# Optimization experiments

Hardware: AMD Instinct MI355X
Metric: run time of the kernel (lower is better)

Reference implementation:

```python
import jax, jax.numpy as jnp
import numpy as np

SCALE = 1.0
DENSE = 4
ITERS = 5


def setup_inputs() -> dict:
    key = jax.random.key(0)
    k1, k2, k3 = jax.random.split(key, 3)
    N, C, H, W = 32, 3, 512, 512
    data = jax.random.uniform(k1, (N, C, H, W), dtype=jnp.float32)
    # marginal attention distributions along x (width) and y (height); strictly positive
    attx = jax.random.uniform(k2, (N, W, 1), dtype=jnp.float32) + 1e-3
    atty = jax.random.uniform(k3, (N, H, 1), dtype=jnp.float32) + 1e-3
    return {"data": data, "attx": attx, "atty": atty}


def _iterative_clip(ax, ay, out_size, dense, iters):
    # ax, ay: (N, A) positive marginals. Normalize so each sums to out_size,
    # then iteratively clip peaks to a threshold and redistribute the clipped
    # mass uniformly (the mobula AttSamplerGrid iterative refinement).
    A = ax.shape[1]
    ax = ax / jnp.sum(ax, 1, keepdims=True) * out_size
    ay = ay / jnp.sum(ay, 1, keepdims=True) * out_size
    thr0 = jnp.float32(dense * out_size / A)
    for i in range(iters):
        t = jnp.minimum(jnp.max(ax, 1, keepdims=True), jnp.max(ay, 1, keepdims=True))
        if i == 0:
            t = jnp.minimum(t, thr0)
        ax = jnp.minimum(ax, t)
        ay = jnp.minimum(ay, t)
        ax = ax + (out_size - jnp.sum(ax, 1, keepdims=True)) / A
        ay = ay + (out_size - jnp.sum(ay, 1, keepdims=True)) / A
    return ax, ay


def _inverse_cdf(att, out_size):
    # att: (N, A) density summing (approximately) to out_size.
    # For each of out_size equally-spaced mass targets, find the fractional
    # source index p (piecewise-linear inverse of the cumulative sum), then
    # map p in [0, A] to a normalized grid coordinate in [-1, 1].
    N, A = att.shape
    c = jnp.cumsum(att, axis=1)                               # (N, A)
    step = c[:, -1] / out_size                                # ~1.0 per output pixel
    t = (jnp.arange(out_size, dtype=att.dtype) + 0.5) * step[:, None]  # (N, out)
    j = jax.vmap(lambda cr, tr: jnp.searchsorted(cr, tr, side="left"))(c, t)
    j = jnp.clip(j, 0, A - 1)
    c_prev = jnp.where(j > 0, jnp.take_along_axis(c, jnp.maximum(j - 1, 0), 1), 0.0)
    dens = jnp.take_along_axis(c, j, 1) - c_prev              # = att[n, j]
    p = j.astype(att.dtype) + (t - c_prev) / jnp.maximum(dens, 1e-6)
    return 2.0 * p / A - 1.0                                  # (N, out) in [-1, 1]


def _grid_sample_bilinear(data, grid):
    # data: (N, C, H, W); grid: (N, Ho, Wo, 2) with grid[...,0]=x, grid[...,1]=y
    # in [-1, 1]; bilinear, align_corners=True, border clamp (grid stays in range).
    N, C, H, W = data.shape
    ix = (grid[..., 0] + 1.0) * 0.5 * (W - 1)
    iy = (grid[..., 1] + 1.0) * 0.5 * (H - 1)
    x0 = jnp.floor(ix)
    y0 = jnp.floor(iy)
    wx = ix - x0
    wy = iy - y0
    x0i = jnp.clip(x0.astype(jnp.int32), 0, W - 1)
    x1i = jnp.clip(x0i + 1, 0, W - 1)
    y0i = jnp.clip(y0.astype(jnp.int32), 0, H - 1)
    y1i = jnp.clip(y0i + 1, 0, H - 1)

    def sample_one(img, x0i, x1i, y0i, y1i, wx, wy):
        # img: (C, H, W); index arrays: (Ho, Wo) -> gathers are (C, Ho, Wo)
        v00 = img[:, y0i, x0i]
        v01 = img[:, y0i, x1i]
        v10 = img[:, y1i, x0i]
        v11 = img[:, y1i, x1i]
        top = v00 * (1.0 - wx) + v01 * wx
        bot = v10 * (1.0 - wx) + v11 * wx
        return top * (1.0 - wy) + bot * wy

    return jax.vmap(sample_one)(data, x0i, x1i, y0i, y1i, wx, wy)


def reference(data, attx, atty):
    N, C, H, W = data.shape
    out_size = int(H * SCALE)
    ax, ay = _iterative_clip(attx[:, :, 0], atty[:, :, 0], out_size, DENSE, ITERS)
    px = _inverse_cdf(ax, out_size)   # x coords, vary along width
    py = _inverse_cdf(ay, out_size)   # y coords, vary along height
    gx = jnp.broadcast_to(px[:, None, :], (N, out_size, out_size))
    gy = jnp.broadcast_to(py[:, :, None], (N, out_size, out_size))
    grid = jnp.stack([gx, gy], axis=3)            # (N, Ho, Wo, 2)
    sampled = _grid_sample_bilinear(data, grid)   # (N, C, Ho, Wo)
    return sampled, grid
```

## Files before the change

kernel.cpp:

```cpp
#include <hip/hip_runtime.h>

#define NB   32
#define NC   3
#define HH   512
#define WW   512
#define AA   512
#define OUT  512

__device__ __forceinline__ void wave_sum2(float& x, float& y) {
#pragma unroll
    for (int m = 32; m > 0; m >>= 1) {
        x += __shfl_xor(x, m, 64);
        y += __shfl_xor(y, m, 64);
    }
}
__device__ __forceinline__ void wave_max2(float& x, float& y) {
#pragma unroll
    for (int m = 32; m > 0; m >>= 1) {
        x = fmaxf(x, __shfl_xor(x, m, 64));
        y = fmaxf(y, __shfl_xor(y, m, 64));
    }
}

__device__ __forceinline__ void block_sum2(float& vx, float& vy,
                                           float* redx, float* redy, int tid) {
    wave_sum2(vx, vy);
    if ((tid & 63) == 0) { redx[tid >> 6] = vx; redy[tid >> 6] = vy; }
    __syncthreads();
    float rx = redx[0], ry = redy[0];
#pragma unroll
    for (int k = 1; k < 8; ++k) { rx += redx[k]; ry += redy[k]; }
    __syncthreads();
    vx = rx; vy = ry;
}
__device__ __forceinline__ void block_max2(float& vx, float& vy,
                                           float* redx, float* redy, int tid) {
    wave_max2(vx, vy);
    if ((tid & 63) == 0) { redx[tid >> 6] = vx; redy[tid >> 6] = vy; }
    __syncthreads();
    float rx = redx[0], ry = redy[0];
#pragma unroll
    for (int k = 1; k < 8; ++k) { rx = fmaxf(rx, redx[k]); ry = fmaxf(ry, redy[k]); }
    __syncthreads();
    vx = rx; vy = ry;
}

__global__ __launch_bounds__(512) void clip_cdf_kernel(
    const float* __restrict__ attx, const float* __restrict__ atty,
    float* __restrict__ px, float* __restrict__ py)
{
    __shared__ float redx[8], redy[8];
    __shared__ float csx[AA], csy[AA];

    const int n    = blockIdx.x;
    const int tid  = threadIdx.x;
    const int wave = tid >> 6;
    const int lane = tid & 63;

    float ax = attx[n * AA + tid];
    float ay = atty[n * AA + tid];

    float sx = ax, sy = ay;
    block_sum2(sx, sy, redx, redy, tid);
    ax = ax / sx * (float)OUT;
    ay = ay / sy * (float)OUT;

#pragma unroll
    for (int it = 0; it < 5; ++it) {
        float mx = ax, my = ay;
        block_max2(mx, my, redx, redy, tid);
        float tv = fminf(mx, my);
        if (it == 0) tv = fminf(tv, 4.0f);
        ax = fminf(ax, tv);
        ay = fminf(ay, tv);
        float sax = ax, say = ay;
        block_sum2(sax, say, redx, redy, tid);
        ax += ((float)OUT - sax) * (1.0f / (float)AA);
        ay += ((float)OUT - say) * (1.0f / (float)AA);
    }

    float vsx = ax, vsy = ay;
#pragma unroll
    for (int off = 1; off < 64; off <<= 1) {
        float ux = __shfl_up(vsx, off, 64);
        float uy = __shfl_up(vsy, off, 64);
        if (lane >= off) { vsx += ux; vsy += uy; }
    }
    if (lane == 63) { redx[wave] = vsx; redy[wave] = vsy; }
    __syncthreads();
    float pfx = 0.0f, pfy = 0.0f;
#pragma unroll
    for (int k = 0; k < 8; ++k) {
        if (k < wave) { pfx += redx[k]; pfy += redy[k]; }
    }
    csx[tid] = vsx + pfx;
    csy[tid] = vsy + pfy;
    __syncthreads();

    const float totx = csx[AA - 1];
    const float toty = csy[AA - 1];
    const float tkx  = ((float)tid + 0.5f) * (totx * (1.0f / (float)OUT));
    const float tky  = ((float)tid + 0.5f) * (toty * (1.0f / (float)OUT));

    {
        int lo = 0, hi = AA;
        while (lo < hi) {
            int mid = (lo + hi) >> 1;
            if (csx[mid] < tkx) lo = mid + 1; else hi = mid;
        }
        int j = min(lo, AA - 1);
        float cprev = (j > 0) ? csx[j - 1] : 0.0f;
        float dens  = csx[j] - cprev;
        float p     = (float)j + (tkx - cprev) / fmaxf(dens, 1e-6f);
        px[n * OUT + tid] = 2.0f * p * (1.0f / (float)AA) - 1.0f;
    }
    {
        int lo = 0, hi = AA;
        while (lo < hi) {
            int mid = (lo + hi) >> 1;
            if (csy[mid] < tky) lo = mid + 1; else hi = mid;
        }
        int j = min(lo, AA - 1);
        float cprev = (j > 0) ? csy[j - 1] : 0.0f;
        float dens  = csy[j] - cprev;
        float p     = (float)j + (tky - cprev) / fmaxf(dens, 1e-6f);
        py[n * OUT + tid] = 2.0f * p * (1.0f / (float)AA) - 1.0f;
    }
}

__global__ __launch_bounds__(256) void sample_kernel(
    const float* __restrict__ data, const float* __restrict__ px,
    const float* __restrict__ py, float* __restrict__ sampled,
    float2* __restrict__ grid)
{
    __shared__ float lrow[6][WW];

    const int d = blockIdx.x;
    const int g = ((d & 7) << 11) + (d >> 3);
    const int n = g >> 9;
    const int i = g & (OUT - 1);

    const float gy  = py[n * OUT + i];
    const float iy  = (gy + 1.0f) * 0.5f * (float)(HH - 1);
    const float y0f = floorf(iy);
    const float wy  = iy - y0f;
    int y0 = (int)y0f;
    y0 = max(0, min(y0, HH - 1));
    const int y1 = min(y0 + 1, HH - 1);

    const float* dbase = data + (size_t)n * NC * HH * WW;

#pragma unroll
    for (int k = 0; k < 3; ++k) {
        const int idx = threadIdx.x + k * 256;
        const int row = idx >> 7;
        const int q   = idx & 127;
        const int c   = (row < 3) ? row : row - 3;
        const int y   = (row < 3) ? y0 : y1;
        const float4 v = ((const float4*)(dbase + ((size_t)c * HH + y) * WW))[q];
        ((float4*)&lrow[row][0])[q] = v;
    }
    __syncthreads();

    float*  sbase  = sampled + (size_t)n * NC * HH * WW + (size_t)i * WW;
    float4* gbase4 = (float4*)(grid + ((size_t)n * OUT + i) * OUT);
    const float omwy = 1.0f - wy;

    const int t = threadIdx.x;
    const float2 pxv = ((const float2*)(px + n * OUT))[t];

    const float ixa  = (pxv.x + 1.0f) * 0.5f * (float)(WW - 1);
    const float x0fa = floorf(ixa);
    const float wxa  = ixa - x0fa;
    int x0a = (int)x0fa; x0a = max(0, min(x0a, WW - 1));
    const int x1a = min(x0a + 1, WW - 1);
    const float omwxa = 1.0f - wxa;
    const float ixb  = (pxv.y + 1.0f) * 0.5f * (float)(WW - 1);
    const float x0fb = floorf(ixb);
    const float wxb  = ixb - x0fb;
    int x0b = (int)x0fb; x0b = max(0, min(x0b, WW - 1));
    const int x1b = min(x0b + 1, WW - 1);
    const float omwxb = 1.0f - wxb;

    gbase4[t] = make_float4(pxv.x, gy, pxv.y, gy);

#pragma unroll
    for (int c = 0; c < NC; ++c) {
        const float* r0 = &lrow[c][0];
        const float* r1 = &lrow[3 + c][0];
        const float topa = r0[x0a] * omwxa + r0[x1a] * wxa;
        const float bota = r1[x0a] * omwxa + r1[x1a] * wxa;
        const float topb = r0[x0b] * omwxb + r0[x1b] * wxb;
        const float botb = r1[x0b] * omwxb + r1[x1b] * wxb;
        const float ra = topa * omwy + bota * wy;
        const float rb = topb * omwy + botb * wy;
        ((float2*)(sbase + (size_t)c * HH * WW))[t] = make_float2(ra, rb);
    }
}

extern "C" void kernel_launch(void* const* d_in, const int* in_sizes, int n_in,
                              void* d_out, int out_size, void* d_ws, size_t ws_size,
                              hipStream_t stream) {
    const float* data = (const float*)d_in[0];
    const float* attx = (const float*)d_in[1];
    const float* atty = (const float*)d_in[2];

    float* px = (float*)d_ws;
    float* py = px + NB * OUT;

    float*  out     = (float*)d_out;
    float*  sampled = out;
    float2* grid    = (float2*)(out + (size_t)NB * NC * HH * WW);

    clip_cdf_kernel<<<NB, 512, 0, stream>>>(attx, atty, px, py);
    sample_kernel<<<NB * OUT, 256, 0, stream>>>(data, px, py, sampled, grid);
}
```

Baseline: 253.8 us.

## Use single-wave clip/CDF kernel and per-channel thread mapping in sampler

The clip/CDF preprocessing kernel becomes a single 64-lane wave in which each lane holds 8 elements. Reductions and the prefix scan then need only shuffles, which removes the block-level barriers, but each lane now runs 16 serial binary searches. The sample kernel goes from 256 to 384 threads so that each thread handles one channel and four output pixels, writing sampled values as float4. The grid write moves to the first 256 threads. The aim is to cut barrier latency in the small kernel and widen the stores in the bandwidth-bound sampler.

```diff
diff --git a/kernel.cpp b/kernel.cpp
--- a/kernel.cpp
+++ b/kernel.cpp
@@ -7,128 +7,134 @@
 #define AA   512
 #define OUT  512
 
-__device__ __forceinline__ void wave_sum2(float& x, float& y) {
-#pragma unroll
-    for (int m = 32; m > 0; m >>= 1) {
-        x += __shfl_xor(x, m, 64);
-        y += __shfl_xor(y, m, 64);
-    }
-}
-__device__ __forceinline__ void wave_max2(float& x, float& y) {
-#pragma unroll
-    for (int m = 32; m > 0; m >>= 1) {
-        x = fmaxf(x, __shfl_xor(x, m, 64));
-        y = fmaxf(y, __shfl_xor(y, m, 64));
-    }
-}
-
-__device__ __forceinline__ void block_sum2(float& vx, float& vy,
-                                           float* redx, float* redy, int tid) {
-    wave_sum2(vx, vy);
-    if ((tid & 63) == 0) { redx[tid >> 6] = vx; redy[tid >> 6] = vy; }
-    __syncthreads();
-    float rx = redx[0], ry = redy[0];
-#pragma unroll
-    for (int k = 1; k < 8; ++k) { rx += redx[k]; ry += redy[k]; }
-    __syncthreads();
-    vx = rx; vy = ry;
-}
-__device__ __forceinline__ void block_max2(float& vx, float& vy,
-                                           float* redx, float* redy, int tid) {
-    wave_max2(vx, vy);
-    if ((tid & 63) == 0) { redx[tid >> 6] = vx; redy[tid >> 6] = vy; }
-    __syncthreads();
-    float rx = redx[0], ry = redy[0];
-#pragma unroll
-    for (int k = 1; k < 8; ++k) { rx = fmaxf(rx, redx[k]); ry = fmaxf(ry, redy[k]); }
-    __syncthreads();
-    vx = rx; vy = ry;
-}
-
-__global__ __launch_bounds__(512) void clip_cdf_kernel(
+__global__ __launch_bounds__(64) void clip_cdf_wave(
     const float* __restrict__ attx, const float* __restrict__ atty,
     float* __restrict__ px, float* __restrict__ py)
 {
-    __shared__ float redx[8], redy[8];
     __shared__ float csx[AA], csy[AA];
-
     const int n    = blockIdx.x;
-    const int tid  = threadIdx.x;
-    const int wave = tid >> 6;
-    const int lane = tid & 63;
-
-    float ax = attx[n * AA + tid];
-    float ay = atty[n * AA + tid];
-
-    float sx = ax, sy = ay;
-    block_sum2(sx, sy, redx, redy, tid);
-    ax = ax / sx * (float)OUT;
-    ay = ay / sy * (float)OUT;
+    const int lane = threadIdx.x;
+
+    float ax[8], ay[8];
+    {
+        const float4* ap = (const float4*)(attx + n * AA);
+        const float4* bp = (const float4*)(atty + n * AA);
+        float4 a0 = ap[lane * 2], a1 = ap[lane * 2 + 1];
+        float4 b0 = bp[lane * 2], b1 = bp[lane * 2 + 1];
+        ax[0]=a0.x; ax[1]=a0.y; ax[2]=a0.z; ax[3]=a0.w;
+        ax[4]=a1.x; ax[5]=a1.y; ax[6]=a1.z; ax[7]=a1.w;
+        ay[0]=b0.x; ay[1]=b0.y; ay[2]=b0.z; ay[3]=b0.w;
+        ay[4]=b1.x; ay[5]=b1.y; ay[6]=b1.z; ay[7]=b1.w;
+    }
+
+    float sx = 0.0f, sy = 0.0f;
+#pragma unroll
+    for (int j = 0; j < 8; ++j) { sx += ax[j]; sy += ay[j]; }
+#pragma unroll
+    for (int m = 32; m > 0; m >>= 1) {
+        sx += __shfl_xor(sx, m, 64);
+        sy += __shfl_xor(sy, m, 64);
+    }
+    const float scx = (float)OUT / sx;
+    const float scy = (float)OUT / sy;
+#pragma unroll
+    for (int j = 0; j < 8; ++j) { ax[j] *= scx; ay[j] *= scy; }
 
 #pragma unroll
     for (int it = 0; it < 5; ++it) {
-        float mx = ax, my = ay;
-        block_max2(mx, my, redx, redy, tid);
+        float mx = ax[0], my = ay[0];
+#pragma unroll
+        for (int j = 1; j < 8; ++j) { mx = fmaxf(mx, ax[j]); my = fmaxf(my, ay[j]); }
+#pragma unroll
+        for (int m = 32; m > 0; m >>= 1) {
+            mx = fmaxf(mx, __shfl_xor(mx, m, 64));
+            my = fmaxf(my, __shfl_xor(my, m, 64));
+        }
         float tv = fminf(mx, my);
         if (it == 0) tv = fminf(tv, 4.0f);
-        ax = fminf(ax, tv);
-        ay = fminf(ay, tv);
-        float sax = ax, say = ay;
-        block_sum2(sax, say, redx, redy, tid);
-        ax += ((float)OUT - sax) * (1.0f / (float)AA);
-        ay += ((float)OUT - say) * (1.0f / (float)AA);
-    }
-
-    float vsx = ax, vsy = ay;
+        float sax = 0.0f, say = 0.0f;
+#pragma unroll
+        for (int j = 0; j < 8; ++j) {
+            ax[j] = fminf(ax[j], tv);  sax += ax[j];
+            ay[j] = fminf(ay[j], tv);  say += ay[j];
+        }
+#pragma unroll
+        for (int m = 32; m > 0; m >>= 1) {
+            sax += __shfl_xor(sax, m, 64);
+            say += __shfl_xor(say, m, 64);
+        }
+        const float dx = ((float)OUT - sax) * (1.0f / (float)AA);
+        const float dy = ((float)OUT - say) * (1.0f / (float)AA);
+#pragma unroll
+        for (int j = 0; j < 8; ++j) { ax[j] += dx; ay[j] += dy; }
+    }
+
+    float psx[8], psy[8];
+    float tx = 0.0f, ty = 0.0f;
+#pragma unroll
+    for (int j = 0; j < 8; ++j) {
+        tx += ax[j]; psx[j] = tx;
+        ty += ay[j]; psy[j] = ty;
+    }
+    float inx = tx, iny = ty;
 #pragma unroll
     for (int off = 1; off < 64; off <<= 1) {
-        float ux = __shfl_up(vsx, off, 64);
-        float uy = __shfl_up(vsy, off, 64);
-        if (lane >= off) { vsx += ux; vsy += uy; }
-    }
-    if (lane == 63) { redx[wave] = vsx; redy[wave] = vsy; }
+        float ux = __shfl_up(inx, off, 64);
+        float uy = __shfl_up(iny, off, 64);
+        if (lane >= off) { inx += ux; iny += uy; }
+    }
+    const float exx = inx - tx;
+    const float exy = iny - ty;
+    const float totx = __shfl(inx, 63, 64);
+    const float toty = __shfl(iny, 63, 64);
+
+    ((float4*)csx)[lane * 2]     = make_float4(exx+psx[0], exx+psx[1], exx+psx[2], exx+psx[3]);
+    ((float4*)csx)[lane * 2 + 1] = make_float4(exx+psx[4], exx+psx[5], exx+psx[6], exx+psx[7]);
+    ((float4*)csy)[lane * 2]     = make_float4(exy+psy[0], exy+psy[1], exy+psy[2], exy+psy[3]);
+    ((float4*)csy)[lane * 2 + 1] = make_float4(exy+psy[4], exy+psy[5], exy+psy[6], exy+psy[7]);
     __syncthreads();
-    float pfx = 0.0f, pfy = 0.0f;
-#pragma unroll
-    for (int k = 0; k < 8; ++k) {
-        if (k < wave) { pfx += redx[k]; pfy += redy[k]; }
-    }
-    csx[tid] = vsx + pfx;
-    csy[tid] = vsy + pfy;
-    __syncthreads();
-
-    const float totx = csx[AA - 1];
-    const float toty = csy[AA - 1];
-    const float tkx  = ((float)tid + 0.5f) * (totx * (1.0f / (float)OUT));
-    const float tky  = ((float)tid + 0.5f) * (toty * (1.0f / (float)OUT));
-
-    {
-        int lo = 0, hi = AA;
-        while (lo < hi) {
-            int mid = (lo + hi) >> 1;
-            if (csx[mid] < tkx) lo = mid + 1; else hi = mid;
-        }
-        int j = min(lo, AA - 1);
-        float cprev = (j > 0) ? csx[j - 1] : 0.0f;
-        float dens  = csx[j] - cprev;
-        float p     = (float)j + (tkx - cprev) / fmaxf(dens, 1e-6f);
-        px[n * OUT + tid] = 2.0f * p * (1.0f / (float)AA) - 1.0f;
-    }
-    {
-        int lo = 0, hi = AA;
-        while (lo < hi) {
-            int mid = (lo + hi) >> 1;
-            if (csy[mid] < tky) lo = mid + 1; else hi = mid;
-        }
-        int j = min(lo, AA - 1);
-        float cprev = (j > 0) ? csy[j - 1] : 0.0f;
-        float dens  = csy[j] - cprev;
-        float p     = (float)j + (tky - cprev) / fmaxf(dens, 1e-6f);
-        py[n * OUT + tid] = 2.0f * p * (1.0f / (float)AA) - 1.0f;
-    }
+
+    const float stx = totx * (1.0f / (float)OUT);
+    const float sty = toty * (1.0f / (float)OUT);
+
+    float outx[8], outy[8];
+#pragma unroll
+    for (int j = 0; j < 8; ++j) {
+        const int t = lane * 8 + j;
+        {
+            const float tk = ((float)t + 0.5f) * stx;
+            int lo = 0, hi = AA;
+            while (lo < hi) {
+                int mid = (lo + hi) >> 1;
+                if (csx[mid] < tk) lo = mid + 1; else hi = mid;
+            }
+            int jj = min(lo, AA - 1);
+            float cprev = (jj > 0) ? csx[jj - 1] : 0.0f;
+            float dens  = csx[jj] - cprev;
+            float p     = (float)jj + (tk - cprev) / fmaxf(dens, 1e-6f);
+            outx[j] = 2.0f * p * (1.0f / (float)AA) - 1.0f;
+        }
+        {
+            const float tk = ((float)t + 0.5f) * sty;
+            int lo = 0, hi = AA;
+            while (lo < hi) {
+                int mid = (lo + hi) >> 1;
+                if (csy[mid] < tk) lo = mid + 1; else hi = mid;
+            }
+            int jj = min(lo, AA - 1);
+            float cprev = (jj > 0) ? csy[jj - 1] : 0.0f;
+            float dens  = csy[jj] - cprev;
+            float p     = (float)jj + (tk - cprev) / fmaxf(dens, 1e-6f);
+            outy[j] = 2.0f * p * (1.0f / (float)AA) - 1.0f;
+        }
+    }
+    ((float4*)(px + n * OUT))[lane * 2]     = make_float4(outx[0], outx[1], outx[2], outx[3]);
+    ((float4*)(px + n * OUT))[lane * 2 + 1] = make_float4(outx[4], outx[5], outx[6], outx[7]);
+    ((float4*)(py + n * OUT))[lane * 2]     = make_float4(outy[0], outy[1], outy[2], outy[3]);
+    ((float4*)(py + n * OUT))[lane * 2 + 1] = make_float4(outy[4], outy[5], outy[6], outy[7]);
 }
 
-__global__ __launch_bounds__(256) void sample_kernel(
+__global__ __launch_bounds__(384) void sample_kernel(
     const float* __restrict__ data, const float* __restrict__ px,
     const float* __restrict__ py, float* __restrict__ sampled,
     float2* __restrict__ grid)
@@ -149,52 +155,50 @@
     const int y1 = min(y0 + 1, HH - 1);
 
     const float* dbase = data + (size_t)n * NC * HH * WW;
-
-#pragma unroll
-    for (int k = 0; k < 3; ++k) {
-        const int idx = threadIdx.x + k * 256;
+    const int tid = threadIdx.x;
+
+#pragma unroll
+    for (int k = 0; k < 2; ++k) {
+        const int idx = tid + k * 384;
         const int row = idx >> 7;
         const int q   = idx & 127;
         const int c   = (row < 3) ? row : row - 3;
         const int y   = (row < 3) ? y0 : y1;
-        const float4 v = ((const float4*)(dbase + ((size_t)c * HH + y) * WW))[q];
-        ((float4*)&lrow[row][0])[q] = v;
+        ((float4*)&lrow[row][0])[q] =
+            ((const float4*)(dbase + ((size_t)c * HH + y) * WW))[q];
     }
     __syncthreads();
 
-    float*  sbase  = sampled + (size_t)n * NC * HH * WW + (size_t)i * WW;
-    float4* gbase4 = (float4*)(grid + ((size_t)n * OUT + i) * OUT);
-    const float omwy = 1.0f - wy;
-
-    const int t = threadIdx.x;
-    const float2 pxv = ((const float2*)(px + n * OUT))[t];
-
-    const float ixa  = (pxv.x + 1.0f) * 0.5f * (float)(WW - 1);
-    const float x0fa = floorf(ixa);
-    const float wxa  = ixa - x0fa;
-    int x0a = (int)x0fa; x0a = max(0, min(x0a, WW - 1));
-    const int x1a = min(x0a + 1, WW - 1);
-    const float omwxa = 1.0f - wxa;
-    const float ixb  = (pxv.y + 1.0f) * 0.5f * (float)(WW - 1);
-    const float x0fb = floorf(ixb);
-    const float wxb  = ixb - x0fb;
-    int x0b = (int)x0fb; x0b = max(0, min(x0b, WW - 1));
-    const int x1b = min(x0b + 1, WW - 1);
-    const float omwxb = 1.0f - wxb;
-
-    gbase4[t] = make_float4(pxv.x, gy, pxv.y, gy);
-
-#pragma unroll
-    for (int c = 0; c < NC; ++c) {
-        const float* r0 = &lrow[c][0];
-        const float* r1 = &lrow[3 + c][0];
-        const float topa = r0[x0a] * omwxa + r0[x1a] * wxa;
-        const float bota = r1[x0a] * omwxa + r1[x1a] * wxa;
-        const float topb = r0[x0b] * omwxb + r0[x1b] * wxb;
-        const float botb = r1[x0b] * omwxb + r1[x1b] * wxb;
-        const float ra = topa * omwy + bota * wy;
-        const float rb = topb * omwy + botb * wy;
-        ((float2*)(sbase + (size_t)c * HH * WW))[t] = make_float2(ra, rb);
+    const int   c  = tid >> 7;
+    const int   gq = tid & 127;
+    const float4 pv = ((const float4*)(px + n * OUT))[gq];
+    const float pxv[4] = { pv.x, pv.y, pv.z, pv.w };
+
+    const float* r0 = &lrow[c][0];
+    const float* r1 = &lrow[3 + c][0];
+
+    float res[4];
+#pragma unroll
+    for (int u = 0; u < 4; ++u) {
+        const float ix  = (pxv[u] + 1.0f) * 0.5f * (float)(WW - 1);
+        const float x0f = floorf(ix);
+        const float wx  = ix - x0f;
+        int x0 = (int)x0f; x0 = max(0, min(x0, WW - 1));
+        const int x1 = min(x0 + 1, WW - 1);
+        const float a0 = r0[x0], a1 = r0[x1];
+        const float b0 = r1[x0], b1 = r1[x1];
+        const float top = a0 + wx * (a1 - a0);
+        const float bot = b0 + wx * (b1 - b0);
+        res[u] = top + wy * (bot - top);
+    }
+    float* sbase = sampled + (size_t)n * NC * HH * WW
+                 + (size_t)c * HH * WW + (size_t)i * WW;
+    ((float4*)sbase)[gq] = make_float4(res[0], res[1], res[2], res[3]);
+
+    if (tid < 256) {
+        const float2 p2 = ((const float2*)(px + n * OUT))[tid];
+        float4* gb = (float4*)(grid + ((size_t)n * OUT + i) * OUT);
+        gb[tid] = make_float4(p2.x, gy, p2.y, gy);
     }
 }
 
@@ -212,6 +216,6 @@
     float*  sampled = out;
     float2* grid    = (float2*)(out + (size_t)NB * NC * HH * WW);
 
-    clip_cdf_kernel<<<NB, 512, 0, stream>>>(attx, atty, px, py);
-    sample_kernel<<<NB * OUT, 256, 0, stream>>>(data, px, py, sampled, grid);
+    clip_cdf_wave<<<NB, 64, 0, stream>>>(attx, atty, px, py);
+    sample_kernel<<<NB * OUT, 384, 0, stream>>>(data, px, py, sampled, grid);
 }
```

New measurement: 260.5 us. 1.03x slower.
